# Performance work log

Hardware: AMD Instinct MI355X
Metric: run time of the kernel (lower is better)

The kernel has to match this reference:

```python
import jax, jax.numpy as jnp
import numpy as np


def setup_inputs() -> dict:
    key = jax.random.key(0)
    ks = jax.random.split(key, 5)
    bt, c, h, w = 64, 64, 32, 32
    x = jax.random.normal(ks[0], (bt, c, h, w), dtype=jnp.float32)
    qkv_w = jax.random.normal(ks[1], (3 * c, c), dtype=jnp.float32) * 0.05
    qkv_b = jax.random.normal(ks[2], (3 * c,), dtype=jnp.float32) * 0.05
    tqk_w = jax.random.normal(ks[3], (2 * c, c, 3, 1, 1), dtype=jnp.float32) * 0.05
    tqk_b = jax.random.normal(ks[4], (2 * c,), dtype=jnp.float32) * 0.05
    return {"x": x, "qkv_w": qkv_w, "qkv_b": qkv_b,
            "tqk_w": tqk_w, "tqk_b": tqk_b, "n_segment": 8}


def reference(x, qkv_w, qkv_b, tqk_w, tqk_b, n_segment):
    bt, c, h, w = x.shape
    t = n_segment
    b = bt // t
    n = h * w
    scale = c ** (-0.5)

    # 1x1 conv -> qkv, then tokens: [bt, n, c]
    qkv = jnp.einsum('bchw,oc->bohw', x, qkv_w) + qkv_b[None, :, None, None]
    q, k, v = jnp.split(qkv, 3, axis=1)
    q, k, v = (a.transpose(0, 2, 3, 1).reshape(bt, n, c) for a in (q, k, v))

    # pixel (spatial) attention over n tokens
    pixel_dots = jnp.einsum('bic,bjc->bij', q, k) * scale          # [bt, n, n]
    pixel_attn = jax.nn.softmax(pixel_dots, axis=-1)
    pixel_out = jnp.einsum('bij,bjd->bid', pixel_attn, v)          # [bt, n, c]

    # channel attention over c channels
    chan_dots = jnp.einsum('bic,bik->bck', q, k) * scale           # [bt, c, c]
    chan_attn = jax.nn.softmax(chan_dots, axis=-1)
    chan_out = jnp.einsum('bij,bdj->bdi', chan_attn, v)            # [bt, n, c]

    x_hat = pixel_out + chan_out                                   # [bt, n, c]
    # '(b t) (h w) c -> b c t h w'
    x_hat = x_hat.reshape(b, t, h, w, c).transpose(0, 4, 1, 2, 3)

    # Conv3d kernel (3,1,1), padding (1,0,0): temporal-only conv
    t_qk = jax.lax.conv_general_dilated(
        x_hat, tqk_w, window_strides=(1, 1, 1),
        padding=[(1, 1), (0, 0), (0, 0)],
        dimension_numbers=('NCDHW', 'OIDHW', 'NCDHW'))
    t_qk = t_qk + tqk_b[None, :, None, None, None]                 # [b, 2c, t, h, w]
    tq, tk = jnp.split(t_qk, 2, axis=1)
    # 'b c t h w -> b t (c h w)'
    tq = tq.transpose(0, 2, 1, 3, 4).reshape(b, t, c * n)
    tk = tk.transpose(0, 2, 1, 3, 4).reshape(b, t, c * n)
    # tv: '(b t) (h w) c -> b t (c h w)'
    tv = v.reshape(b, t, h, w, c).transpose(0, 1, 4, 2, 3).reshape(b, t, c * n)

    dots = jnp.einsum('bid,bjd->bij', tq, tk)                      # [b, t, t] (no scale, as source)
    attn = jax.nn.softmax(dots, axis=-1)
    out = jnp.einsum('bkt,btd->bkd', attn, tv)                     # [b, t, c*n]
    out = out.reshape(b, t, c, h, w).reshape(bt, c, h, w)
    return out
```

## Files before the change

kernel.cpp:

```cpp
#include <hip/hip_runtime.h>

#define SCALE 0.125f

typedef _Float16 f16;
typedef _Float16 f16x2 __attribute__((ext_vector_type(2)));
typedef _Float16 f16x8 __attribute__((ext_vector_type(8)));
typedef float f32x4 __attribute__((ext_vector_type(4)));

#define MFMA16(A,B,C) __builtin_amdgcn_mfma_f32_16x16x32_f16(A,B,C,0,0,0)

__device__ __forceinline__ float dp4(const float a[4], const float b[4], float acc) {
    acc = fmaf(a[0], b[0], acc);
    acc = fmaf(a[1], b[1], acc);
    acc = fmaf(a[2], b[2], acc);
    acc = fmaf(a[3], b[3], acc);
    return acc;
}

__device__ __forceinline__ int sw(int row) {
    return ((row & 7) ^ ((row >> 3) & 7)) << 4;
}

__global__ __launch_bounds__(256) void k_qkv(const float* __restrict__ x,
                                             const float* __restrict__ w,
                                             const float* __restrict__ bias,
                                             const float* __restrict__ tqkw,
                                             f16* __restrict__ q,
                                             f16* __restrict__ k,
                                             f16* __restrict__ v,
                                             f16* __restrict__ vt,
                                             f16* __restrict__ wsplit) {
    const int tid = threadIdx.x;
    if (blockIdx.y == 64) {
#pragma unroll
        for (int it = 0; it < 6; ++it) {
            int d = blockIdx.x * 1536 + it * 256 + tid;
            int j = d & 7, oc = (d >> 3) & 127, kg = (d >> 10) & 3, kc = d >> 12;
            int K = kc * 32 + kg * 8 + j;
            int dt = K >> 6, ci = K & 63;
            float wf = tqkw[(oc * 64 + ci) * 3 + dt];
            f16 h = (f16)wf;
            wsplit[d] = h;
            wsplit[24576 + d] = (f16)(wf - (float)h);
        }
        return;
    }
    __shared__ float xs[64][64];
    __shared__ float ws[192][65];
    __shared__ f16 vts[4096];
    const int bt = blockIdx.y, pos0 = blockIdx.x * 64;

    for (int it = 0; it < 16; ++it) {
        int idx = it * 256 + tid;
        int ci = idx >> 6, p = idx & 63;
        xs[ci][p] = x[(bt * 64 + ci) * 1024 + pos0 + p];
    }
    for (int it = 0; it < 48; ++it) {
        int idx = it * 256 + tid;
        ws[idx / 64][idx % 64] = w[idx];
    }
    __syncthreads();

    const int oc = tid & 63, grp = tid >> 6;
    float accq[16], acck[16], accv[16];
    const float bq = bias[oc], bk = bias[64 + oc], bv = bias[128 + oc];
#pragma unroll
    for (int p = 0; p < 16; ++p) { accq[p] = bq; acck[p] = bk; accv[p] = bv; }

    for (int ci = 0; ci < 64; ++ci) {
        float wq = ws[oc][ci], wk = ws[64 + oc][ci], wv = ws[128 + oc][ci];
        const float4* xr = (const float4*)&xs[ci][grp * 16];
#pragma unroll
        for (int p4 = 0; p4 < 4; ++p4) {
            float xa[4];
            *(float4*)xa = xr[p4];
#pragma unroll
            for (int e = 0; e < 4; ++e) {
                int p = p4 * 4 + e;
                accq[p] = fmaf(wq, xa[e], accq[p]);
                acck[p] = fmaf(wk, xa[e], acck[p]);
                accv[p] = fmaf(wv, xa[e], accv[p]);
            }
        }
    }
#pragma unroll
    for (int p = 0; p < 16; ++p) {
        int pos = pos0 + grp * 16 + p;
        int base = (bt * 1024 + pos) * 64 + oc;
        f16 vh = (f16)accv[p];
        q[base] = (f16)(accq[p] * SCALE);
        k[base] = (f16)acck[p];
        v[base] = vh;
        int col = grp * 16 + p;
        *(f16*)((char*)vts + oc * 128 + ((col * 2) ^ sw(oc))) = vh;
    }
    __syncthreads();
#pragma unroll
    for (int it = 0; it < 2; ++it) {
        int s = it * 256 + tid;
        int row = s >> 3, c8 = s & 7;
        f16x8 val = *(const f16x8*)((char*)vts + row * 128 + ((c8 * 16) ^ sw(row)));
        *(f16x8*)(vt + (bt * 64 + row) * 1024 + pos0 + c8 * 8) = val;
    }
}

__global__ __launch_bounds__(256) void k_chan_part(const f16* __restrict__ q,
                                                   const f16* __restrict__ k,
                                                   float* __restrict__ partials) {
    __shared__ float qs[64][68];
    __shared__ float ks[64][68];
    const int pc = blockIdx.x, bt = blockIdx.y, tid = threadIdx.x;
    const int ti = tid >> 4, tj = tid & 15;
    float acc[4][4] = {{0.f}};

    for (int ch = 0; ch < 4; ++ch) {
        int p0 = pc * 256 + ch * 64;
        __syncthreads();
        for (int it = 0; it < 2; ++it) {
            int e8 = it * 256 + tid;
            int p = e8 >> 3, c8 = e8 & 7;
            f16x8 qv = *(const f16x8*)(q + (bt * 1024 + p0 + p) * 64 + c8 * 8);
            f16x8 kv = *(const f16x8*)(k + (bt * 1024 + p0 + p) * 64 + c8 * 8);
            float4 qlo = make_float4((float)qv[0], (float)qv[1], (float)qv[2], (float)qv[3]);
            float4 qhi = make_float4((float)qv[4], (float)qv[5], (float)qv[6], (float)qv[7]);
            float4 klo = make_float4((float)kv[0], (float)kv[1], (float)kv[2], (float)kv[3]);
            float4 khi = make_float4((float)kv[4], (float)kv[5], (float)kv[6], (float)kv[7]);
            *(float4*)&qs[p][c8 * 8]     = qlo;
            *(float4*)&qs[p][c8 * 8 + 4] = qhi;
            *(float4*)&ks[p][c8 * 8]     = klo;
            *(float4*)&ks[p][c8 * 8 + 4] = khi;
        }
        __syncthreads();
#pragma unroll 8
        for (int p = 0; p < 64; ++p) {
            float qa[4], ka[4];
            *(float4*)qa = *(const float4*)&qs[p][ti * 4];
            *(float4*)ka = *(const float4*)&ks[p][tj * 4];
#pragma unroll
            for (int r = 0; r < 4; ++r)
#pragma unroll
                for (int c = 0; c < 4; ++c)
                    acc[r][c] = fmaf(qa[r], ka[c], acc[r][c]);
        }
    }
#pragma unroll
    for (int r = 0; r < 4; ++r) {
        float4 o4 = make_float4(acc[r][0], acc[r][1], acc[r][2], acc[r][3]);
        *(float4*)&partials[((bt * 4 + pc) * 64 + ti * 4 + r) * 64 + tj * 4] = o4;
    }
}

__global__ __launch_bounds__(256) void k_chan_red(const float* __restrict__ partials,
                                                  f16* __restrict__ cattn) {
    const int bt = blockIdx.x, tid = threadIdx.x;
    const int i = tid >> 2, q4 = tid & 3;
    float s[16];
#pragma unroll
    for (int jj = 0; jj < 16; ++jj) s[jj] = 0.f;
#pragma unroll
    for (int pc = 0; pc < 4; ++pc) {
        const float4* src = (const float4*)(partials + ((bt * 4 + pc) * 64 + i) * 64 + q4 * 16);
#pragma unroll
        for (int f4 = 0; f4 < 4; ++f4) {
            float a[4];
            *(float4*)a = src[f4];
#pragma unroll
            for (int e = 0; e < 4; ++e) s[f4 * 4 + e] += a[e];
        }
    }
    float m = -1e30f;
#pragma unroll
    for (int jj = 0; jj < 16; ++jj) m = fmaxf(m, s[jj]);
    m = fmaxf(m, __shfl_xor(m, 1, 64));
    m = fmaxf(m, __shfl_xor(m, 2, 64));
    float e[16], sum = 0.f;
#pragma unroll
    for (int jj = 0; jj < 16; ++jj) { e[jj] = __expf(s[jj] - m); sum += e[jj]; }
    sum += __shfl_xor(sum, 1, 64);
    sum += __shfl_xor(sum, 2, 64);
    float inv = 1.f / sum;
    f16x8 o0, o1;
#pragma unroll
    for (int jj = 0; jj < 8; ++jj) { o0[jj] = (f16)(e[jj] * inv); o1[jj] = (f16)(e[8 + jj] * inv); }
    f16* dst = cattn + (bt * 64 + i) * 64 + q4 * 16;
    *(f16x8*)dst = o0;
    *(f16x8*)(dst + 8) = o1;
}

__global__ __launch_bounds__(256) void k_pixel(const f16* __restrict__ q,
                                               const f16* __restrict__ k,
                                               const f16* __restrict__ v,
                                               const f16* __restrict__ vt,
                                               const f16* __restrict__ cattn,
                                               f16* __restrict__ xh,
                                               f16* __restrict__ xl) {
    __shared__ f16 kv_s[2][8192];
    __shared__ char p_raw[18432];

    const int bt = blockIdx.x, row0 = blockIdx.y * 128;
    const int tid = threadIdx.x;
    const int wv = tid >> 6;
    const int ln = tid & 15;
    const int kgrp = (tid >> 4) & 3;
    const int r2 = tid >> 3, c8 = tid & 7;

    f16x8 k0, k1, v0, v1;
    const f16* kbase = k + bt * 1024 * 64;
    const f16* vtbase = vt + (size_t)bt * 65536;

    auto issue = [&](int ch) {
        const f16* kg = kbase + ch * 64 * 64;
        const f16* vtg = vtbase + ch * 64;
        k0 = *(const f16x8*)(kg + r2 * 64 + c8 * 8);
        k1 = *(const f16x8*)(kg + (r2 + 32) * 64 + c8 * 8);
        v0 = *(const f16x8*)(vtg + r2 * 1024 + c8 * 8);
        v1 = *(const f16x8*)(vtg + (r2 + 32) * 1024 + c8 * 8);
    };
    auto commit = [&](int buf) {
        char* kb = (char*)&kv_s[buf][0];
        char* vb = (char*)&kv_s[buf][4096];
        *(f16x8*)(kb + r2 * 128 + ((c8 * 16) ^ sw(r2))) = k0;
        *(f16x8*)(kb + (r2 + 32) * 128 + ((c8 * 16) ^ sw(r2 + 32))) = k1;
        *(f16x8*)(vb + r2 * 128 + ((c8 * 16) ^ sw(r2))) = v0;
        *(f16x8*)(vb + (r2 + 32) * 128 + ((c8 * 16) ^ sw(r2 + 32))) = v1;
    };

    issue(0);
    {
        const f16* qg = q + (bt * 1024 + row0) * 64;
#pragma unroll
        for (int p = 0; p < 4; ++p) {
            int e8 = p * 256 + tid;
            int rr = e8 >> 3, cc = e8 & 7;
            f16x8 val = *(const f16x8*)(qg + rr * 64 + cc * 8);
            *(f16x8*)(p_raw + rr * 128 + ((cc * 16) ^ sw(rr))) = val;
        }
    }
    __syncthreads();
    f16x8 qa[2][2];
#pragma unroll
    for (int rt = 0; rt < 2; ++rt) {
        int rr = rt * 64 + 16 * wv + ln;
#pragma unroll
        for (int kb = 0; kb < 2; ++kb)
            qa[rt][kb] = *(const f16x8*)(p_raw + rr * 128 + (((kb * 4 + kgrp) * 16) ^ sw(rr)));
    }
    commit(0);
    issue(1);
    __syncthreads();

    f32x4 out[2][4];
    float lr[2] = {0.f, 0.f};
#pragma unroll
    for (int rt = 0; rt < 2; ++rt)
#pragma unroll
        for (int ct = 0; ct < 4; ++ct) out[rt][ct] = (f32x4){0.f, 0.f, 0.f, 0.f};

    for (int ch = 0; ch < 16; ++ch) {
        const char* kb = (const char*)&kv_s[ch & 1][0];
        const char* vb = (const char*)&kv_s[ch & 1][4096];

        f16x8 kf[4][2];
#pragma unroll
        for (int jt = 0; jt < 4; ++jt)
#pragma unroll
            for (int kb2 = 0; kb2 < 2; ++kb2) {
                int jr = jt * 16 + ln;
                kf[jt][kb2] = *(const f16x8*)(kb + jr * 128 + (((kb2 * 4 + kgrp) * 16) ^ sw(jr)));
            }
#pragma unroll
        for (int rt = 0; rt < 2; ++rt) {
            int prow = rt * 64 + wv * 16 + ln;
            char* pb = p_raw + prow * 144;
            f32x4 sx[4];
#pragma unroll
            for (int jt = 0; jt < 4; ++jt) sx[jt] = (f32x4){0.f, 0.f, 0.f, 0.f};
#pragma unroll
            for (int jt = 0; jt < 4; ++jt)
#pragma unroll
                for (int kb2 = 0; kb2 < 2; ++kb2)
                    sx[jt] = MFMA16(kf[jt][kb2], qa[rt][kb2], sx[jt]);
#pragma unroll
            for (int jt = 0; jt < 4; ++jt) {
                float p0 = __expf(sx[jt][0]), p1 = __expf(sx[jt][1]);
                float p2 = __expf(sx[jt][2]), p3 = __expf(sx[jt][3]);
                lr[rt] += (p0 + p1) + (p2 + p3);
                f16x2 w0, w1;
                w0[0] = (f16)p0; w0[1] = (f16)p1;
                w1[0] = (f16)p2; w1[1] = (f16)p3;
                *(f16x2*)(pb + (jt * 8 + kgrp * 2) * 4) = w0;
                *(f16x2*)(pb + (jt * 8 + kgrp * 2 + 1) * 4) = w1;
            }
        }
        f16x8 vf[4][2];
#pragma unroll
        for (int ct = 0; ct < 4; ++ct)
#pragma unroll
            for (int kb2 = 0; kb2 < 2; ++kb2) {
                int cr = ct * 16 + ln;
                vf[ct][kb2] = *(const f16x8*)(vb + cr * 128 + (((kb2 * 4 + kgrp) * 16) ^ sw(cr)));
            }
#pragma unroll
        for (int rt = 0; rt < 2; ++rt) {
            int prow = rt * 64 + wv * 16 + ln;
            f16x8 pa[2];
#pragma unroll
            for (int kb2 = 0; kb2 < 2; ++kb2)
                pa[kb2] = *(const f16x8*)(p_raw + prow * 144 + (kb2 * 16 + kgrp * 4) * 4);
#pragma unroll
            for (int ct = 0; ct < 4; ++ct)
#pragma unroll
                for (int kb2 = 0; kb2 < 2; ++kb2)
                    out[rt][ct] = MFMA16(pa[kb2], vf[ct][kb2], out[rt][ct]);
        }
        if (ch < 15) {
            commit((ch + 1) & 1);
            if (ch < 14) issue(ch + 2);
        }
        __syncthreads();
    }

    float invr[2][4];
#pragma unroll
    for (int rt = 0; rt < 2; ++rt) {
        float l = lr[rt];
        l += __shfl_xor(l, 16, 64);
        l += __shfl_xor(l, 32, 64);
        float inv = 1.f / l;
#pragma unroll
        for (int r = 0; r < 4; ++r)
            invr[rt][r] = __shfl(inv, kgrp * 4 + r, 64);
#pragma unroll
        for (int r = 0; r < 4; ++r)
#pragma unroll
            for (int ct = 0; ct < 4; ++ct) out[rt][ct][r] *= invr[rt][r];
    }

    {
        f16* cs = &kv_s[0][0];
        const f16* cg = cattn + bt * 4096;
#pragma unroll
        for (int p = 0; p < 2; ++p) {
            int e8 = p * 256 + tid;
            int rr = e8 >> 3, cc = e8 & 7;
            f16x8 cv = *(const f16x8*)(cg + rr * 64 + cc * 8);
            *(f16x8*)((char*)cs + rr * 128 + ((cc * 16) ^ sw(rr))) = cv;
        }
        const f16* vg = v + (bt * 1024 + row0) * 64;
#pragma unroll
        for (int p = 0; p < 4; ++p) {
            int e8 = p * 256 + tid;
            int rr = e8 >> 3, cc = e8 & 7;
            f16x8 vv = *(const f16x8*)(vg + rr * 64 + cc * 8);
            *(f16x8*)(p_raw + rr * 128 + ((cc * 16) ^ sw(rr))) = vv;
        }
    }
    __syncthreads();
    {
        const char* cs = (const char*)&kv_s[0][0];
        f16x8 cb[4][2];
#pragma unroll
        for (int it = 0; it < 4; ++it)
#pragma unroll
            for (int kb2 = 0; kb2 < 2; ++kb2) {
                int ir = it * 16 + ln;
                cb[it][kb2] = *(const f16x8*)(cs + ir * 128 + (((kb2 * 4 + kgrp) * 16) ^ sw(ir)));
            }
#pragma unroll
        for (int rt = 0; rt < 2; ++rt) {
            int rr = rt * 64 + 16 * wv + ln;
            f16x8 va[2];
#pragma unroll
            for (int kb2 = 0; kb2 < 2; ++kb2)
                va[kb2] = *(const f16x8*)(p_raw + rr * 128 + (((kb2 * 4 + kgrp) * 16) ^ sw(rr)));
#pragma unroll
            for (int it = 0; it < 4; ++it)
#pragma unroll
                for (int kb2 = 0; kb2 < 2; ++kb2)
                    out[rt][it] = MFMA16(va[kb2], cb[it][kb2], out[rt][it]);
        }
    }

#pragma unroll
    for (int rt = 0; rt < 2; ++rt)
#pragma unroll
        for (int ct = 0; ct < 4; ++ct)
#pragma unroll
            for (int r = 0; r < 4; ++r) {
                float val = out[rt][ct][r];
                f16 h = (f16)val;
                int idx = (bt * 1024 + row0 + rt * 64 + 16 * wv + kgrp * 4 + r) * 64 + ct * 16 + ln;
                xh[idx] = h;
                xl[idx] = (f16)(val - (float)h);
            }
}

__global__ __launch_bounds__(256) void k_tconv(const f16* __restrict__ xh,
                                               const f16* __restrict__ xl,
                                               const f16* __restrict__ wsplit,
                                               const float* __restrict__ bias,
                                               float* __restrict__ tq,
                                               float* __restrict__ tk) {
    __shared__ f16 xs[2][3][4096];
    const int bt = blockIdx.y, pos0 = blockIdx.x * 64;
    const int b = bt >> 3, t = bt & 7;
    const int tid = threadIdx.x;
    const int wvid = tid >> 6, ln = tid & 15, kgrp = (tid >> 4) & 3;

    for (int dt = 0; dt < 3; ++dt) {
        int tt = t + dt - 1;
        bool ok = (tt >= 0) && (tt < 8);
        const f16* srch = xh + ((b * 8 + tt) * 1024 + pos0) * 64;
        const f16* srcl = xl + ((b * 8 + tt) * 1024 + pos0) * 64;
#pragma unroll
        for (int p = 0; p < 2; ++p) {
            int e8 = p * 256 + tid;
            int r2 = e8 >> 3, c8 = e8 & 7;
            f16x8 vh = {0, 0, 0, 0, 0, 0, 0, 0};
            f16x8 vl = {0, 0, 0, 0, 0, 0, 0, 0};
            if (ok) {
                vh = *(const f16x8*)(srch + r2 * 64 + c8 * 8);
                vl = *(const f16x8*)(srcl + r2 * 64 + c8 * 8);
            }
            int byte = r2 * 128 + ((c8 * 16) ^ sw(r2));
            *(f16x8*)((char*)&xs[0][dt][0] + byte) = vh;
            *(f16x8*)((char*)&xs[1][dt][0] + byte) = vl;
        }
    }

    f16x8 bh[2][6], bl[2][6];
#pragma unroll
    for (int og = 0; og < 2; ++og) {
        int oc = wvid * 32 + og * 16 + ln;
#pragma unroll
        for (int kc = 0; kc < 6; ++kc) {
            int idx = (kc * 4 + kgrp) * 1024 + oc * 8;
            bh[og][kc] = *(const f16x8*)(wsplit + idx);
            bl[og][kc] = *(const f16x8*)(wsplit + 24576 + idx);
        }
    }
    __syncthreads();

#pragma unroll
    for (int pg = 0; pg < 4; ++pg) {
        f16x8 ah[6], al[6];
        int rr = pg * 16 + ln;
#pragma unroll
        for (int kc = 0; kc < 6; ++kc) {
            int dt = kc >> 1;
            int ci0 = (kc & 1) * 32 + kgrp * 8;
            int byte = rr * 128 + ((ci0 * 2) ^ sw(rr));
            ah[kc] = *(const f16x8*)((char*)&xs[0][dt][0] + byte);
            al[kc] = *(const f16x8*)((char*)&xs[1][dt][0] + byte);
        }
#pragma unroll
        for (int og = 0; og < 2; ++og) {
            int oc = wvid * 32 + og * 16 + ln;
            float bv = bias[oc];
            f32x4 acc = {bv, bv, bv, bv};
#pragma unroll
            for (int kc = 0; kc < 6; ++kc) {
                acc = MFMA16(ah[kc], bh[og][kc], acc);
                acc = MFMA16(al[kc], bh[og][kc], acc);
                acc = MFMA16(ah[kc], bl[og][kc], acc);
            }
            float* dst = (oc < 64) ? tq : tk;
            int orow = oc & 63;
            int pos = pos0 + pg * 16 + kgrp * 4;
            *(float4*)&dst[(bt * 64 + orow) * 1024 + pos] =
                make_float4(acc[0], acc[1], acc[2], acc[3]);
        }
    }
}

__global__ __launch_bounds__(256) void k_tdots(const float* __restrict__ tq,
                                               const float* __restrict__ tk,
                                               float* __restrict__ partials) {
    __shared__ float qs[8][516];
    __shared__ float ks[8][516];
    const int ch = blockIdx.x, b = blockIdx.y;
    const int tid = threadIdx.x;
    const int d0 = ch * 512;

    for (int it = 0; it < 4; ++it) {
        int f4 = it * 256 + tid;
        int i = f4 >> 7, d4 = f4 & 127;
        *(float4*)&qs[i][d4 * 4] = *(const float4*)(tq + (size_t)(b * 8 + i) * 65536 + d0 + d4 * 4);
        *(float4*)&ks[i][d4 * 4] = *(const float4*)(tk + (size_t)(b * 8 + i) * 65536 + d0 + d4 * 4);
    }
    __syncthreads();

    const int p = tid >> 2, sub = tid & 3;
    const int i = p >> 3, j = p & 7;
    float acc = 0.f;
#pragma unroll 8
    for (int d4 = 0; d4 < 32; ++d4) {
        int off = (d4 * 4 + sub) * 4;
        float qa[4], ka[4];
        *(float4*)qa = *(const float4*)&qs[i][off];
        *(float4*)ka = *(const float4*)&ks[j][off];
        acc = dp4(qa, ka, acc);
    }
    acc += __shfl_xor(acc, 1, 64);
    acc += __shfl_xor(acc, 2, 64);
    if (sub == 0) partials[(b * 128 + ch) * 64 + p] = acc;
}

__global__ __launch_bounds__(256) void k_tout(const f16* __restrict__ v,
                                              const float* __restrict__ partials,
                                              float* __restrict__ outp) {
    __shared__ float sred[32][9];
    __shared__ float ta_s[4][8];
    __shared__ float ot[64][65];
    const int pt = blockIdx.x, kq = blockIdx.y, b = blockIdx.z;
    const int pos0 = pt * 64;
    const int tid = threadIdx.x;

    {
        const int pair = tid & 31, grp8 = tid >> 5;
        const int i = kq * 4 + (pair >> 3), j = pair & 7;
        float s = 0.f;
#pragma unroll
        for (int c = 0; c < 16; ++c)
            s += partials[(b * 128 + grp8 * 16 + c) * 64 + i * 8 + j];
        sred[pair][grp8] = s;
    }
    __syncthreads();
    if (tid < 32) {
        float t = 0.f;
#pragma unroll
        for (int g = 0; g < 8; ++g) t += sred[tid][g];
        float m = t;
        m = fmaxf(m, __shfl_xor(m, 1, 64));
        m = fmaxf(m, __shfl_xor(m, 2, 64));
        m = fmaxf(m, __shfl_xor(m, 4, 64));
        float e = __expf(t - m);
        float se = e;
        se += __shfl_xor(se, 1, 64);
        se += __shfl_xor(se, 2, 64);
        se += __shfl_xor(se, 4, 64);
        ta_s[tid >> 3][tid & 7] = e / se;
    }
    __syncthreads();

    const int cc = tid & 63, grp = tid >> 6;
    float tar[4][8];
#pragma unroll
    for (int kk = 0; kk < 4; ++kk)
#pragma unroll
        for (int t = 0; t < 8; ++t) tar[kk][t] = ta_s[kk][t];
    float acc[4][16];
#pragma unroll
    for (int kk = 0; kk < 4; ++kk)
#pragma unroll
        for (int pp = 0; pp < 16; ++pp) acc[kk][pp] = 0.f;
#pragma unroll
    for (int t = 0; t < 8; ++t) {
        const f16* vb = v + ((size_t)(b * 8 + t) * 1024 + pos0) * 64 + cc;
#pragma unroll
        for (int pp = 0; pp < 16; ++pp) {
            float vv = (float)vb[(grp * 16 + pp) * 64];
#pragma unroll
            for (int kk = 0; kk < 4; ++kk)
                acc[kk][pp] = fmaf(tar[kk][t], vv, acc[kk][pp]);
        }
    }
#pragma unroll
    for (int kk = 0; kk < 4; ++kk) {
        __syncthreads();
#pragma unroll
        for (int pp = 0; pp < 16; ++pp) ot[cc][grp * 16 + pp] = acc[kk][pp];
        __syncthreads();
        float* dst = outp + ((size_t)(b * 8 + kq * 4 + kk) * 64) * 1024 + pos0;
        for (int it = 0; it < 16; ++it) {
            int idx = it * 256 + tid;
            int c2 = idx >> 6, p2 = idx & 63;
            dst[c2 * 1024 + p2] = ot[c2][p2];
        }
    }
}

extern "C" void kernel_launch(void* const* d_in, const int* in_sizes, int n_in,
                              void* d_out, int out_size, void* d_ws, size_t ws_size,
                              hipStream_t stream) {
    const float* x     = (const float*)d_in[0];
    const float* qkv_w = (const float*)d_in[1];
    const float* qkv_b = (const float*)d_in[2];
    const float* tqk_w = (const float*)d_in[3];
    const float* tqk_b = (const float*)d_in[4];
    float* outp = (float*)d_out;

    char* wsb = (char*)d_ws;
    f16*   q        = (f16*)wsb;
    f16*   k        = (f16*)(wsb + (8u << 20));
    f16*   v        = (f16*)(wsb + (16u << 20));
    f16*   cattn    = (f16*)(wsb + (24u << 20));
    float* tpart    = (float*)(wsb + (24u << 20) + (1u << 19));
    f16*   wsplit   = (f16*)(wsb + (24u << 20) + (1u << 19) + (1u << 18) + 8192);
    f16*   xhat_hi  = (f16*)(wsb + (25u << 20));
    f16*   xhat_lo  = (f16*)(wsb + (33u << 20));
    float* cpart    = (float*)(wsb + (41u << 20));
    float* tq       = (float*)wsb;
    float* tk       = (float*)(wsb + (41u << 20));
    f16*   vt       = (f16*)(wsb + (57u << 20));

    k_qkv      <<<dim3(16, 65), 256, 0, stream>>>(x, qkv_w, qkv_b, tqk_w, q, k, v, vt, wsplit);
    k_chan_part<<<dim3(4, 64), 256, 0, stream>>>(q, k, cpart);
    k_chan_red <<<dim3(64), 256, 0, stream>>>(cpart, cattn);
    k_pixel    <<<dim3(64, 8), 256, 0, stream>>>(q, k, v, vt, cattn, xhat_hi, xhat_lo);
    k_tconv    <<<dim3(16, 64), 256, 0, stream>>>(xhat_hi, xhat_lo, wsplit, tqk_b, tq, tk);
    k_tdots    <<<dim3(128, 8), 256, 0, stream>>>(tq, tk, tpart);
    k_tout     <<<dim3(16, 2, 8), 256, 0, stream>>>(v, tpart, outp);
}
```

Measured before the change: 178.3 us.

## Fuse temporal conv with temporal dot products and swizzle pixel P tile

```diff
diff --git a/kernel.cpp b/kernel.cpp
--- a/kernel.cpp
+++ b/kernel.cpp
@@ -195,7 +195,7 @@
                                                f16* __restrict__ xh,
                                                f16* __restrict__ xl) {
     __shared__ f16 kv_s[2][8192];
-    __shared__ char p_raw[18432];
+    __shared__ char p_raw[16384];
 
     const int bt = blockIdx.x, row0 = blockIdx.y * 128;
     const int tid = threadIdx.x;
@@ -271,7 +271,8 @@
 #pragma unroll
         for (int rt = 0; rt < 2; ++rt) {
             int prow = rt * 64 + wv * 16 + ln;
-            char* pb = p_raw + prow * 144;
+            char* pb = p_raw + prow * 128;
+            const int swz = sw(prow);
             f32x4 sx[4];
 #pragma unroll
             for (int jt = 0; jt < 4; ++jt) sx[jt] = (f32x4){0.f, 0.f, 0.f, 0.f};
@@ -288,8 +289,9 @@
                 f16x2 w0, w1;
                 w0[0] = (f16)p0; w0[1] = (f16)p1;
                 w1[0] = (f16)p2; w1[1] = (f16)p3;
-                *(f16x2*)(pb + (jt * 8 + kgrp * 2) * 4) = w0;
-                *(f16x2*)(pb + (jt * 8 + kgrp * 2 + 1) * 4) = w1;
+                int base = (jt * 32 + kgrp * 8) ^ swz;
+                *(f16x2*)(pb + base) = w0;
+                *(f16x2*)(pb + base + 4) = w1;
             }
         }
         f16x8 vf[4][2];
@@ -303,10 +305,11 @@
 #pragma unroll
         for (int rt = 0; rt < 2; ++rt) {
             int prow = rt * 64 + wv * 16 + ln;
+            const int swz = sw(prow);
             f16x8 pa[2];
 #pragma unroll
             for (int kb2 = 0; kb2 < 2; ++kb2)
-                pa[kb2] = *(const f16x8*)(p_raw + prow * 144 + (kb2 * 16 + kgrp * 4) * 4);
+                pa[kb2] = *(const f16x8*)(p_raw + prow * 128 + ((kb2 * 64 + kgrp * 16) ^ swz));
 #pragma unroll
             for (int ct = 0; ct < 4; ++ct)
 #pragma unroll
@@ -395,38 +398,18 @@
             }
 }
 
-__global__ __launch_bounds__(256) void k_tconv(const f16* __restrict__ xh,
-                                               const f16* __restrict__ xl,
-                                               const f16* __restrict__ wsplit,
-                                               const float* __restrict__ bias,
-                                               float* __restrict__ tq,
-                                               float* __restrict__ tk) {
-    __shared__ f16 xs[2][3][4096];
-    const int bt = blockIdx.y, pos0 = blockIdx.x * 64;
-    const int b = bt >> 3, t = bt & 7;
+__global__ __launch_bounds__(256) void k_tcd(const f16* __restrict__ xh,
+                                             const f16* __restrict__ xl,
+                                             const f16* __restrict__ wsplit,
+                                             const float* __restrict__ bias,
+                                             float* __restrict__ partials) {
+    extern __shared__ char lds[];
+    float* tqs = (float*)lds;
+    float* tks = (float*)(lds + 66560);
+    f16*   xst = (f16*)(lds + 133120);
+    const int pt = blockIdx.x, b = blockIdx.y;
     const int tid = threadIdx.x;
     const int wvid = tid >> 6, ln = tid & 15, kgrp = (tid >> 4) & 3;
-
-    for (int dt = 0; dt < 3; ++dt) {
-        int tt = t + dt - 1;
-        bool ok = (tt >= 0) && (tt < 8);
-        const f16* srch = xh + ((b * 8 + tt) * 1024 + pos0) * 64;
-        const f16* srcl = xl + ((b * 8 + tt) * 1024 + pos0) * 64;
-#pragma unroll
-        for (int p = 0; p < 2; ++p) {
-            int e8 = p * 256 + tid;
-            int r2 = e8 >> 3, c8 = e8 & 7;
-            f16x8 vh = {0, 0, 0, 0, 0, 0, 0, 0};
-            f16x8 vl = {0, 0, 0, 0, 0, 0, 0, 0};
-            if (ok) {
-                vh = *(const f16x8*)(srch + r2 * 64 + c8 * 8);
-                vl = *(const f16x8*)(srcl + r2 * 64 + c8 * 8);
-            }
-            int byte = r2 * 128 + ((c8 * 16) ^ sw(r2));
-            *(f16x8*)((char*)&xs[0][dt][0] + byte) = vh;
-            *(f16x8*)((char*)&xs[1][dt][0] + byte) = vl;
-        }
-    }
 
     f16x8 bh[2][6], bl[2][6];
 #pragma unroll
@@ -439,71 +422,112 @@
             bl[og][kc] = *(const f16x8*)(wsplit + 24576 + idx);
         }
     }
-    __syncthreads();
-
-#pragma unroll
-    for (int pg = 0; pg < 4; ++pg) {
-        f16x8 ah[6], al[6];
-        int rr = pg * 16 + ln;
-#pragma unroll
-        for (int kc = 0; kc < 6; ++kc) {
-            int dt = kc >> 1;
-            int ci0 = (kc & 1) * 32 + kgrp * 8;
-            int byte = rr * 128 + ((ci0 * 2) ^ sw(rr));
-            ah[kc] = *(const f16x8*)((char*)&xs[0][dt][0] + byte);
-            al[kc] = *(const f16x8*)((char*)&xs[1][dt][0] + byte);
-        }
-#pragma unroll
-        for (int og = 0; og < 2; ++og) {
-            int oc = wvid * 32 + og * 16 + ln;
-            float bv = bias[oc];
-            f32x4 acc = {bv, bv, bv, bv};
+
+    const int srow = tid >> 3, sc8 = tid & 7;
+    auto stage = [&](int tt) {
+        int s = tt % 3;
+        size_t goff = ((size_t)(b * 8 + tt) * 1024 + pt * 32 + srow) * 64 + sc8 * 8;
+        f16x8 vh = *(const f16x8*)(xh + goff);
+        f16x8 vl = *(const f16x8*)(xl + goff);
+        int byte = srow * 128 + ((sc8 * 16) ^ sw(srow));
+        *(f16x8*)((char*)(xst + s * 2048) + byte) = vh;
+        *(f16x8*)((char*)(xst + (3 + s) * 2048) + byte) = vl;
+    };
+
+    stage(0);
+    for (int t = 0; t < 8; ++t) {
+        if (t + 1 < 8) stage(t + 1);
+        __syncthreads();
+#pragma unroll
+        for (int pg = 0; pg < 2; ++pg) {
+            f16x8 ah[6], al[6];
+            bool valid[6];
+            int rr = pg * 16 + ln;
 #pragma unroll
             for (int kc = 0; kc < 6; ++kc) {
-                acc = MFMA16(ah[kc], bh[og][kc], acc);
-                acc = MFMA16(al[kc], bh[og][kc], acc);
-                acc = MFMA16(ah[kc], bl[og][kc], acc);
-            }
-            float* dst = (oc < 64) ? tq : tk;
-            int orow = oc & 63;
-            int pos = pos0 + pg * 16 + kgrp * 4;
-            *(float4*)&dst[(bt * 64 + orow) * 1024 + pos] =
-                make_float4(acc[0], acc[1], acc[2], acc[3]);
-        }
-    }
-}
-
-__global__ __launch_bounds__(256) void k_tdots(const float* __restrict__ tq,
-                                               const float* __restrict__ tk,
-                                               float* __restrict__ partials) {
-    __shared__ float qs[8][516];
-    __shared__ float ks[8][516];
-    const int ch = blockIdx.x, b = blockIdx.y;
-    const int tid = threadIdx.x;
-    const int d0 = ch * 512;
-
-    for (int it = 0; it < 4; ++it) {
-        int f4 = it * 256 + tid;
-        int i = f4 >> 7, d4 = f4 & 127;
-        *(float4*)&qs[i][d4 * 4] = *(const float4*)(tq + (size_t)(b * 8 + i) * 65536 + d0 + d4 * 4);
-        *(float4*)&ks[i][d4 * 4] = *(const float4*)(tk + (size_t)(b * 8 + i) * 65536 + d0 + d4 * 4);
-    }
-    __syncthreads();
-
-    const int p = tid >> 2, sub = tid & 3;
-    const int i = p >> 3, j = p & 7;
-    float acc = 0.f;
-#pragma unroll 8
-    for (int d4 = 0; d4 < 32; ++d4) {
-        int off = (d4 * 4 + sub) * 4;
-        float qa[4], ka[4];
-        *(float4*)qa = *(const float4*)&qs[i][off];
-        *(float4*)ka = *(const float4*)&ks[j][off];
-        acc = dp4(qa, ka, acc);
-    }
-    acc += __shfl_xor(acc, 1, 64);
-    acc += __shfl_xor(acc, 2, 64);
-    if (sub == 0) partials[(b * 128 + ch) * 64 + p] = acc;
+                int dt = kc >> 1;
+                int tt = t + dt - 1;
+                valid[kc] = (tt >= 0) && (tt < 8);
+                if (valid[kc]) {
+                    int s = tt % 3;
+                    int ci0 = (kc & 1) * 32 + kgrp * 8;
+                    int byte = rr * 128 + ((ci0 * 2) ^ sw(rr));
+                    ah[kc] = *(const f16x8*)((char*)(xst + s * 2048) + byte);
+                    al[kc] = *(const f16x8*)((char*)(xst + (3 + s) * 2048) + byte);
+                } else {
+                    ah[kc] = (f16x8){0,0,0,0,0,0,0,0};
+                    al[kc] = (f16x8){0,0,0,0,0,0,0,0};
+                }
+            }
+#pragma unroll
+            for (int og = 0; og < 2; ++og) {
+                int oc = wvid * 32 + og * 16 + ln;
+                float bv = bias[oc];
+                f32x4 acc = {bv, bv, bv, bv};
+#pragma unroll
+                for (int kc = 0; kc < 6; ++kc) {
+                    if (valid[kc]) {
+                        acc = MFMA16(ah[kc], bh[og][kc], acc);
+                        acc = MFMA16(al[kc], bh[og][kc], acc);
+                        acc = MFMA16(ah[kc], bl[og][kc], acc);
+                    }
+                }
+                float* dst = (oc < 64) ? tqs : tks;
+                int c = oc & 63;
+                int posb = pg * 16 + kgrp * 4;
+#pragma unroll
+                for (int r = 0; r < 4; ++r)
+                    dst[t * 2080 + (posb + r) * 65 + c] = acc[r];
+            }
+        }
+        __syncthreads();
+    }
+
+    const int dpos = tid >> 3, dc0 = (tid & 7) * 8;
+    float tqa[8][8];
+#pragma unroll
+    for (int i = 0; i < 8; ++i) {
+        const float* src = tqs + i * 2080 + dpos * 65 + dc0;
+#pragma unroll
+        for (int e = 0; e < 8; ++e) tqa[i][e] = src[e];
+    }
+    float part[8][8];
+#pragma unroll
+    for (int i = 0; i < 8; ++i)
+#pragma unroll
+        for (int j = 0; j < 8; ++j) part[i][j] = 0.f;
+#pragma unroll
+    for (int j = 0; j < 8; ++j) {
+        float tkb[8];
+        const float* src = tks + j * 2080 + dpos * 65 + dc0;
+#pragma unroll
+        for (int e = 0; e < 8; ++e) tkb[e] = src[e];
+#pragma unroll
+        for (int i = 0; i < 8; ++i)
+#pragma unroll
+            for (int e = 0; e < 8; ++e)
+                part[i][j] = fmaf(tqa[i][e], tkb[e], part[i][j]);
+    }
+    __syncthreads();
+    float* red2 = (float*)lds;
+    float* sred = (float*)(lds + 66560);
+#pragma unroll
+    for (int i = 0; i < 8; ++i)
+#pragma unroll
+        for (int j = 0; j < 8; ++j)
+            red2[(i * 8 + j) * 257 + tid] = part[i][j];
+    __syncthreads();
+    {
+        int pair = tid & 63, q4 = tid >> 6;
+        float s = 0.f;
+        const float* src = red2 + pair * 257 + q4 * 64;
+        for (int c = 0; c < 64; ++c) s += src[c];
+        sred[pair * 4 + q4] = s;
+    }
+    __syncthreads();
+    if (tid < 64)
+        partials[(b * 32 + pt) * 64 + tid] =
+            sred[tid * 4] + sred[tid * 4 + 1] + sred[tid * 4 + 2] + sred[tid * 4 + 3];
 }
 
 __global__ __launch_bounds__(256) void k_tout(const f16* __restrict__ v,
@@ -521,8 +545,8 @@
         const int i = kq * 4 + (pair >> 3), j = pair & 7;
         float s = 0.f;
 #pragma unroll
-        for (int c = 0; c < 16; ++c)
-            s += partials[(b * 128 + grp8 * 16 + c) * 64 + i * 8 + j];
+        for (int c = 0; c < 4; ++c)
+            s += partials[(b * 32 + grp8 * 4 + c) * 64 + i * 8 + j];
         sred[pair][grp8] = s;
     }
     __syncthreads();
@@ -600,15 +624,15 @@
     f16*   xhat_hi  = (f16*)(wsb + (25u << 20));
     f16*   xhat_lo  = (f16*)(wsb + (33u << 20));
     float* cpart    = (float*)(wsb + (41u << 20));
-    float* tq       = (float*)wsb;
-    float* tk       = (float*)(wsb + (41u << 20));
     f16*   vt       = (f16*)(wsb + (57u << 20));
+
+    hipFuncSetAttribute((const void*)k_tcd,
+                        hipFuncAttributeMaxDynamicSharedMemorySize, 157696);
 
     k_qkv      <<<dim3(16, 65), 256, 0, stream>>>(x, qkv_w, qkv_b, tqk_w, q, k, v, vt, wsplit);
     k_chan_part<<<dim3(4, 64), 256, 0, stream>>>(q, k, cpart);
     k_chan_red <<<dim3(64), 256, 0, stream>>>(cpart, cattn);
     k_pixel    <<<dim3(64, 8), 256, 0, stream>>>(q, k, v, vt, cattn, xhat_hi, xhat_lo);
-    k_tconv    <<<dim3(16, 64), 256, 0, stream>>>(xhat_hi, xhat_lo, wsplit, tqk_b, tq, tk);
-    k_tdots    <<<dim3(128, 8), 256, 0, stream>>>(tq, tk, tpart);
+    k_tcd      <<<dim3(32, 8), 256, 157696, stream>>>(xhat_hi, xhat_lo, wsplit, tqk_b, tpart);
     k_tout     <<<dim3(16, 2, 8), 256, 0, stream>>>(v, tpart, outp);
 }
```

Result: faster. 165.8 us (-7.0%).
